# Performance work log

Measured on AMD Instinct MI355X. Metric: run time of the kernel, lower is better.

The kernel has to match this reference:

```python
import jax, jax.numpy as jnp
import numpy as np
from jax import lax

H = 64          # GRU hidden size
OUT_STEPS = 20  # output_seq_size


def _maxpool2(x):
    # x: [N, C, H, W] -> 2x2 max pool, stride 2, VALID
    return lax.reduce_window(x, -jnp.inf, lax.max, (1, 1, 2, 2), (1, 1, 2, 2), 'VALID')


def _conv(x, w, b):
    # NCHW / OIHW, VALID, stride 1
    y = lax.conv_general_dilated(x, w, (1, 1), 'VALID',
                                 dimension_numbers=('NCHW', 'OIHW', 'NCHW'))
    return y + b[None, :, None, None]


def _gru_step(h, x, wih, whh, bih, bhh):
    # PyTorch GRU gate order: r, z, n
    gi = x @ wih.T + bih            # [B, 3H]
    gh = h @ whh.T + bhh            # [B, 3H]
    i_r, i_z, i_n = jnp.split(gi, 3, axis=-1)
    h_r, h_z, h_n = jnp.split(gh, 3, axis=-1)
    r = jax.nn.sigmoid(i_r + h_r)
    z = jax.nn.sigmoid(i_z + h_z)
    n = jnp.tanh(i_n + r * h_n)
    return (1.0 - z) * n + z * h


def setup_inputs() -> dict:
    key = jax.random.key(0)
    ks = jax.random.split(key, 20)
    B, T = 1024, 31
    s = 0.1
    return {
        'bbox_seq': jax.random.normal(ks[0], (B, T, 4), jnp.float32),
        'head_seq': jax.random.uniform(ks[1], (B, T, 32, 32), jnp.float32),
        'conv1_w': jax.random.normal(ks[2], (4, 1, 3, 3), jnp.float32) * s,
        'conv1_b': jax.random.normal(ks[3], (4,), jnp.float32) * s,
        'conv2_w': jax.random.normal(ks[4], (10, 4, 3, 3), jnp.float32) * s,
        'conv2_b': jax.random.normal(ks[5], (10,), jnp.float32) * s,
        'fc_w': jax.random.normal(ks[6], (5, 360), jnp.float32) * s,
        'fc_b': jax.random.normal(ks[7], (5,), jnp.float32) * s,
        'enc_wih': jax.random.normal(ks[8], (3 * H, 9), jnp.float32) * s,
        'enc_whh': jax.random.normal(ks[9], (3 * H, H), jnp.float32) * s,
        'enc_bih': jax.random.normal(ks[10], (3 * H,), jnp.float32) * s,
        'enc_bhh': jax.random.normal(ks[11], (3 * H,), jnp.float32) * s,
        'dec_wih': jax.random.normal(ks[12], (3 * H, 4), jnp.float32) * s,
        'dec_whh': jax.random.normal(ks[13], (3 * H, H), jnp.float32) * s,
        'dec_bih': jax.random.normal(ks[14], (3 * H,), jnp.float32) * s,
        'dec_bhh': jax.random.normal(ks[15], (3 * H,), jnp.float32) * s,
        'lin_w': jax.random.normal(ks[16], (4, H), jnp.float32) * s,
        'lin_b': jax.random.normal(ks[17], (4,), jnp.float32) * s,
    }


def reference(bbox_seq, head_seq, conv1_w, conv1_b, conv2_w, conv2_b, fc_w, fc_b,
              enc_wih, enc_whh, enc_bih, enc_bhh,
              dec_wih, dec_whh, dec_bih, dec_bhh, lin_w, lin_b):
    B, T = bbox_seq.shape[0], bbox_seq.shape[1]
    L = T - 1  # encoder sequence length

    # offset: last bbox, broadcast over OUT_STEPS -> [B, OUT_STEPS, 4]
    offset = jnp.broadcast_to(bbox_seq[:, -1][:, None, :], (B, OUT_STEPS, 4))

    diffs = bbox_seq[:, 1:] - bbox_seq[:, :-1]  # [B, L, 4] (dropout p=0 -> identity)

    # --- ConvEncoder on all head crops at once ---
    imgs = head_seq[:, :-1].reshape(B * L, 1, 32, 32)
    x = jax.nn.relu(_conv(imgs, conv1_w, conv1_b))   # [BL, 4, 30, 30]
    x = _maxpool2(x)                                  # [BL, 4, 15, 15]
    x = jax.nn.relu(_conv(x, conv2_w, conv2_b))       # [BL, 10, 13, 13]
    x = _maxpool2(x)                                  # [BL, 10, 6, 6]
    emb = x.reshape(B * L, -1) @ fc_w.T + fc_b        # [BL, 5]
    emb = emb.reshape(B, L, -1)

    enc_in = jnp.concatenate([diffs, emb], axis=2)    # [B, L, 9]

    # --- GRU encoder (scan over time) ---
    def enc_step(h, x_t):
        h = _gru_step(h, x_t, enc_wih, enc_whh, enc_bih, enc_bhh)
        return h, None
    h0 = jnp.zeros((B, H), enc_in.dtype)
    hn, _ = lax.scan(enc_step, h0, jnp.swapaxes(enc_in, 0, 1))

    def dec_step(carry, _):
        h, prev_x = carry
        h = _gru_step(h, prev_x, dec_wih, dec_whh, dec_bih, dec_bhh)
        x_new = h @ lin_w.T + lin_b + prev_x
        return (h, x_new), x_new
    (_, _), outs = lax.scan(dec_step, (hn, diffs[:, -1]), None, length=OUT_STEPS)
    out = jnp.swapaxes(outs, 0, 1)                    # [B, OUT_STEPS, 4]

    return jnp.cumsum(out, axis=1) + offset
```

## Files before the change

### kernel.cpp

```cpp
#include <hip/hip_runtime.h>
#include <hip/hip_bf16.h>


#define B_    1024
#define L_    30
#define H_    64

__device__ __forceinline__ float sigmoid_f(float v) {
    return 1.f / (1.f + __expf(-v));
}
__device__ __forceinline__ float tanh_f(float v) {
    v = fminf(fmaxf(v, -15.f), 15.f);
    float e = __expf(2.f * v);
    return (e - 1.f) / (e + 1.f);
}
__device__ __forceinline__ float bcast(float v, int lane) {
    return __int_as_float(__builtin_amdgcn_readlane(__float_as_int(v), lane));
}
__device__ __forceinline__ void load4_lds(float* r, const float* p) {
    float2 a = *(const float2*)p;
    float2 b = *(const float2*)(p + 2);
    r[0] = a.x; r[1] = a.y; r[2] = b.x; r[3] = b.y;
}

__global__ __launch_bounds__(64) void conv_embed_kernel(
    const float* __restrict__ bbox,
    const float* __restrict__ head,
    const float* __restrict__ c1w, const float* __restrict__ c1b,
    const float* __restrict__ c2w, const float* __restrict__ c2b,
    const float* __restrict__ fcw, const float* __restrict__ fcb,
    float* __restrict__ enc_in)
{
    const int img = blockIdx.x;
    const int b = img / L_;
    const int l = img % L_;
    const int tid = threadIdx.x;

    __shared__ float s_img[32 * 32];
    __shared__ float s_p1[4 * 15 * 16];
    __shared__ float s_p2[360];
    __shared__ float s_red[60];

    {
        const float4* src = (const float4*)(head + ((size_t)b * 31 + (size_t)l) * 1024);
        float4* dst = (float4*)s_img;
        #pragma unroll
        for (int i = 0; i < 4; ++i) dst[tid + 64 * i] = src[tid + 64 * i];
    }
    __syncthreads();

    if (tid < 60) {
        const int c = tid / 15, px = tid % 15;
        const int x0 = 2 * px;
        float w[9];
        #pragma unroll
        for (int k = 0; k < 9; ++k) w[k] = c1w[c * 9 + k];
        const float bias = c1b[c];

        float r0[4], r1[4], r2[4], r3[4];
        load4_lds(r0, s_img + 0 * 32 + x0);
        load4_lds(r1, s_img + 1 * 32 + x0);
        #pragma unroll
        for (int py = 0; py < 15; ++py) {
            load4_lds(r2, s_img + (2 * py + 2) * 32 + x0);
            load4_lds(r3, s_img + (2 * py + 3) * 32 + x0);
            float a00 = bias, a01 = bias, a10 = bias, a11 = bias;
            #pragma unroll
            for (int kx = 0; kx < 3; ++kx) {
                const float w0 = w[kx], w1 = w[3 + kx], w2 = w[6 + kx];
                a00 = fmaf(w0, r0[kx],     fmaf(w1, r1[kx],     fmaf(w2, r2[kx],     a00)));
                a01 = fmaf(w0, r0[kx + 1], fmaf(w1, r1[kx + 1], fmaf(w2, r2[kx + 1], a01)));
                a10 = fmaf(w0, r1[kx],     fmaf(w1, r2[kx],     fmaf(w2, r3[kx],     a10)));
                a11 = fmaf(w0, r1[kx + 1], fmaf(w1, r2[kx + 1], fmaf(w2, r3[kx + 1], a11)));
            }
            a00 = fmaxf(a00, 0.f); a01 = fmaxf(a01, 0.f);
            a10 = fmaxf(a10, 0.f); a11 = fmaxf(a11, 0.f);
            s_p1[c * 240 + py * 16 + px] = fmaxf(fmaxf(a00, a01), fmaxf(a10, a11));
            #pragma unroll
            for (int q = 0; q < 4; ++q) { r0[q] = r2[q]; r1[q] = r3[q]; }
        }
    }
    __syncthreads();

    if (tid < 60) {
        const int c = tid / 6, px = tid % 6;
        const int x0 = 2 * px;
        float w[4][9];
        #pragma unroll
        for (int ic = 0; ic < 4; ++ic)
            #pragma unroll
            for (int k = 0; k < 9; ++k) w[ic][k] = c2w[(c * 4 + ic) * 9 + k];
        const float bias = c2b[c];

        float win[4][4][4];
        #pragma unroll
        for (int ic = 0; ic < 4; ++ic) {
            load4_lds(win[0][ic], s_p1 + ic * 240 + 0 * 16 + x0);
            load4_lds(win[1][ic], s_p1 + ic * 240 + 1 * 16 + x0);
        }
        #pragma unroll
        for (int py = 0; py < 6; ++py) {
            #pragma unroll
            for (int ic = 0; ic < 4; ++ic) {
                load4_lds(win[2][ic], s_p1 + ic * 240 + (2 * py + 2) * 16 + x0);
                load4_lds(win[3][ic], s_p1 + ic * 240 + (2 * py + 3) * 16 + x0);
            }
            float a00 = bias, a01 = bias, a10 = bias, a11 = bias;
            #pragma unroll
            for (int ic = 0; ic < 4; ++ic) {
                #pragma unroll
                for (int kx = 0; kx < 3; ++kx) {
                    const float w0 = w[ic][kx], w1 = w[ic][3 + kx], w2 = w[ic][6 + kx];
                    a00 = fmaf(w0, win[0][ic][kx],     fmaf(w1, win[1][ic][kx],     fmaf(w2, win[2][ic][kx],     a00)));
                    a01 = fmaf(w0, win[0][ic][kx + 1], fmaf(w1, win[1][ic][kx + 1], fmaf(w2, win[2][ic][kx + 1], a01)));
                    a10 = fmaf(w0, win[1][ic][kx],     fmaf(w1, win[2][ic][kx],     fmaf(w2, win[3][ic][kx],     a10)));
                    a11 = fmaf(w0, win[1][ic][kx + 1], fmaf(w1, win[2][ic][kx + 1], fmaf(w2, win[3][ic][kx + 1], a11)));
                }
            }
            a00 = fmaxf(a00, 0.f); a01 = fmaxf(a01, 0.f);
            a10 = fmaxf(a10, 0.f); a11 = fmaxf(a11, 0.f);
            s_p2[c * 36 + py * 6 + px] = fmaxf(fmaxf(a00, a01), fmaxf(a10, a11));
            #pragma unroll
            for (int ic = 0; ic < 4; ++ic)
                #pragma unroll
                for (int q = 0; q < 4; ++q) { win[0][ic][q] = win[2][ic][q]; win[1][ic][q] = win[3][ic][q]; }
        }
    }
    __syncthreads();

    if (tid < 60) {
        const int o = tid / 12, i0 = tid % 12;
        const float* wrow = fcw + o * 360;
        float acc = 0.f;
        #pragma unroll
        for (int k = 0; k < 30; ++k) {
            const int i = i0 + 12 * k;
            acc = fmaf(wrow[i], s_p2[i], acc);
        }
        s_red[tid] = acc;
    }
    __syncthreads();

    float* dst = enc_in + ((size_t)b * L_ + l) * 9;
    if (tid < 5) {
        float acc = fcb[tid];
        #pragma unroll
        for (int k = 0; k < 12; ++k) acc += s_red[tid * 12 + k];
        dst[4 + tid] = acc;
    } else if (tid >= 8 && tid < 12) {
        const int d = tid - 8;
        const float* bb = bbox + (size_t)b * 124 + (size_t)l * 4;
        dst[d] = bb[4 + d] - bb[d];
    }
}

__global__ __launch_bounds__(64, 1) void gru_encdec_kernel(
    const float* __restrict__ bbox,
    const float* __restrict__ enc_in,
    const float* __restrict__ ewih, const float* __restrict__ ewhh,
    const float* __restrict__ ebih, const float* __restrict__ ebhh,
    const float* __restrict__ dwih, const float* __restrict__ dwhh,
    const float* __restrict__ dbih, const float* __restrict__ dbhh,
    const float* __restrict__ linw, const float* __restrict__ linb,
    float* __restrict__ out)
{
    const int b = blockIdx.x;
    const int j = threadIdx.x;

    __shared__ float xs[272];
    for (int i = j; i < 270; i += 64) xs[i] = enc_in[(size_t)b * 270 + i];

    float h = 0.f;

    {
        float Wh[3][64];
        #pragma unroll
        for (int g = 0; g < 3; ++g) {
            const float4* row = (const float4*)(ewhh + (size_t)(g * 64 + j) * 64);
            #pragma unroll
            for (int k4 = 0; k4 < 16; ++k4) *(float4*)&Wh[g][4 * k4] = row[k4];
        }
        float Wi[3][9];
        #pragma unroll
        for (int g = 0; g < 3; ++g) {
            const float* row = ewih + (g * 64 + j) * 9;
            #pragma unroll
            for (int k = 0; k < 9; ++k) Wi[g][k] = row[k];
        }
        const float bi0 = ebih[j], bi1 = ebih[64 + j], bi2 = ebih[128 + j];
        const float bh0 = ebhh[j], bh1 = ebhh[64 + j], bh2 = ebhh[128 + j];

        __syncthreads();

        #pragma unroll 1
        for (int t = 0; t < L_; ++t) {
            float gr = bi0 + bh0, gz = bi1 + bh1, gni = bi2, gnh = bh2;
            #pragma unroll
            for (int k = 0; k < 9; ++k) {
                const float xk = xs[t * 9 + k];
                gr  = fmaf(Wi[0][k], xk, gr);
                gz  = fmaf(Wi[1][k], xk, gz);
                gni = fmaf(Wi[2][k], xk, gni);
            }
            #pragma unroll
            for (int k = 0; k < 64; ++k) {
                const float hk = bcast(h, k);
                gr  = fmaf(Wh[0][k], hk, gr);
                gz  = fmaf(Wh[1][k], hk, gz);
                gnh = fmaf(Wh[2][k], hk, gnh);
            }
            const float r = sigmoid_f(gr);
            const float z = sigmoid_f(gz);
            const float n = tanh_f(gni + r * gnh);
            h = (1.f - z) * n + z * h;
        }
    }

    {
        float Wh[3][64];
        #pragma unroll
        for (int g = 0; g < 3; ++g) {
            const float4* row = (const float4*)(dwhh + (size_t)(g * 64 + j) * 64);
            #pragma unroll
            for (int k4 = 0; k4 < 16; ++k4) *(float4*)&Wh[g][4 * k4] = row[k4];
        }
        float Wi[3][4];
        #pragma unroll
        for (int g = 0; g < 3; ++g) {
            const float* row = dwih + (g * 64 + j) * 4;
            #pragma unroll
            for (int k = 0; k < 4; ++k) Wi[g][k] = row[k];
        }
        const float bi0 = dbih[j], bi1 = dbih[64 + j], bi2 = dbih[128 + j];
        const float bh0 = dbhh[j], bh1 = dbhh[64 + j], bh2 = dbhh[128 + j];
        const float lw0 = linw[j], lw1 = linw[64 + j], lw2 = linw[128 + j], lw3 = linw[192 + j];
        const float lb0 = linb[0], lb1 = linb[1], lb2 = linb[2], lb3 = linb[3];

        const float* bb = bbox + (size_t)b * 124;
        float px0 = bb[120] - bb[116];
        float px1 = bb[121] - bb[117];
        float px2 = bb[122] - bb[118];
        float px3 = bb[123] - bb[119];
        const float of0 = bb[120], of1 = bb[121], of2 = bb[122], of3 = bb[123];
        float cs0 = 0.f, cs1 = 0.f, cs2 = 0.f, cs3 = 0.f;
        float4* outp = (float4*)(out + (size_t)b * 80);

        #pragma unroll 1
        for (int t = 0; t < 20; ++t) {
            float gr = bi0 + bh0, gz = bi1 + bh1, gni = bi2, gnh = bh2;
            gr  = fmaf(Wi[0][0], px0, fmaf(Wi[0][1], px1, fmaf(Wi[0][2], px2, fmaf(Wi[0][3], px3, gr))));
            gz  = fmaf(Wi[1][0], px0, fmaf(Wi[1][1], px1, fmaf(Wi[1][2], px2, fmaf(Wi[1][3], px3, gz))));
            gni = fmaf(Wi[2][0], px0, fmaf(Wi[2][1], px1, fmaf(Wi[2][2], px2, fmaf(Wi[2][3], px3, gni))));
            #pragma unroll
            for (int k = 0; k < 64; ++k) {
                const float hk = bcast(h, k);
                gr  = fmaf(Wh[0][k], hk, gr);
                gz  = fmaf(Wh[1][k], hk, gz);
                gnh = fmaf(Wh[2][k], hk, gnh);
            }
            const float r = sigmoid_f(gr);
            const float z = sigmoid_f(gz);
            const float n = tanh_f(gni + r * gnh);
            h = (1.f - z) * n + z * h;

            float v0 = lw0 * h, v1 = lw1 * h, v2 = lw2 * h, v3 = lw3 * h;
            #pragma unroll
            for (int s = 32; s > 0; s >>= 1) {
                v0 += __shfl_xor(v0, s);
                v1 += __shfl_xor(v1, s);
                v2 += __shfl_xor(v2, s);
                v3 += __shfl_xor(v3, s);
            }
            px0 = v0 + lb0 + px0;
            px1 = v1 + lb1 + px1;
            px2 = v2 + lb2 + px2;
            px3 = v3 + lb3 + px3;
            cs0 += px0; cs1 += px1; cs2 += px2; cs3 += px3;
            if (j == 0) outp[t] = make_float4(cs0 + of0, cs1 + of1, cs2 + of2, cs3 + of3);
        }
    }
}

extern "C" void kernel_launch(void* const* d_in, const int* in_sizes, int n_in,
                              void* d_out, int out_size, void* d_ws, size_t ws_size,
                              hipStream_t stream) {
    (void)in_sizes; (void)n_in; (void)out_size; (void)ws_size;
    const float* bbox = (const float*)d_in[0];
    const float* head = (const float*)d_in[1];
    const float* c1w  = (const float*)d_in[2];
    const float* c1b  = (const float*)d_in[3];
    const float* c2w  = (const float*)d_in[4];
    const float* c2b  = (const float*)d_in[5];
    const float* fcw  = (const float*)d_in[6];
    const float* fcb  = (const float*)d_in[7];
    const float* ewih = (const float*)d_in[8];
    const float* ewhh = (const float*)d_in[9];
    const float* ebih = (const float*)d_in[10];
    const float* ebhh = (const float*)d_in[11];
    const float* dwih = (const float*)d_in[12];
    const float* dwhh = (const float*)d_in[13];
    const float* dbih = (const float*)d_in[14];
    const float* dbhh = (const float*)d_in[15];
    const float* linw = (const float*)d_in[16];
    const float* linb = (const float*)d_in[17];
    float* out = (float*)d_out;

    float* enc_in = (float*)d_ws;

    conv_embed_kernel<<<B_ * L_, 64, 0, stream>>>(bbox, head, c1w, c1b, c2w, c2b,
                                                  fcw, fcb, enc_in);
    gru_encdec_kernel<<<B_, 64, 0, stream>>>(bbox, enc_in,
                                             ewih, ewhh, ebih, ebhh,
                                             dwih, dwhh, dbih, dbhh,
                                             linw, linb, out);
}
```

Baseline: 320.4 us.

## Use fp16 packed dot products for GRU recurrence and rotate conv row buffers

The GRU encoder and decoder recurrent weights are now held as packed half2 registers. The hidden state is broadcast through LDS as fp16 instead of 64 readlane operations, and v_dot2 fp16 instructions accumulate into fp32. This halves the register footprint of the weights and cuts the number of FMAs and broadcasts per step on the serial critical path, at the cost of reduced precision in the recurrence. Separately, the conv1 and conv2 loops use a 6-slot ring buffer of rows so that register copies between iterations are avoided.

```diff
diff --git a/kernel.cpp b/kernel.cpp
--- a/kernel.cpp
+++ b/kernel.cpp
@@ -5,6 +5,9 @@
 #define B_    1024
 #define L_    30
 #define H_    64
+
+typedef _Float16 half_t;
+typedef __attribute__((ext_vector_type(2))) _Float16 half2_t;
 
 __device__ __forceinline__ float sigmoid_f(float v) {
     return 1.f / (1.f + __expf(-v));
@@ -13,9 +16,6 @@
     v = fminf(fmaxf(v, -15.f), 15.f);
     float e = __expf(2.f * v);
     return (e - 1.f) / (e + 1.f);
-}
-__device__ __forceinline__ float bcast(float v, int lane) {
-    return __int_as_float(__builtin_amdgcn_readlane(__float_as_int(v), lane));
 }
 __device__ __forceinline__ void load4_lds(float* r, const float* p) {
     float2 a = *(const float2*)p;
@@ -52,78 +52,96 @@
     if (tid < 60) {
         const int c = tid / 15, px = tid % 15;
         const int x0 = 2 * px;
-        float w[9];
-        #pragma unroll
-        for (int k = 0; k < 9; ++k) w[k] = c1w[c * 9 + k];
+        float wg[9];
+        #pragma unroll
+        for (int k = 0; k < 9; ++k) wg[k] = c1w[c * 9 + k];
         const float bias = c1b[c];
 
-        float r0[4], r1[4], r2[4], r3[4];
-        load4_lds(r0, s_img + 0 * 32 + x0);
-        load4_lds(r1, s_img + 1 * 32 + x0);
-        #pragma unroll
-        for (int py = 0; py < 15; ++py) {
-            load4_lds(r2, s_img + (2 * py + 2) * 32 + x0);
-            load4_lds(r3, s_img + (2 * py + 3) * 32 + x0);
+        auto c1out = [&](const float* ra, const float* rb, const float* rc, const float* rd) -> float {
             float a00 = bias, a01 = bias, a10 = bias, a11 = bias;
             #pragma unroll
             for (int kx = 0; kx < 3; ++kx) {
-                const float w0 = w[kx], w1 = w[3 + kx], w2 = w[6 + kx];
-                a00 = fmaf(w0, r0[kx],     fmaf(w1, r1[kx],     fmaf(w2, r2[kx],     a00)));
-                a01 = fmaf(w0, r0[kx + 1], fmaf(w1, r1[kx + 1], fmaf(w2, r2[kx + 1], a01)));
-                a10 = fmaf(w0, r1[kx],     fmaf(w1, r2[kx],     fmaf(w2, r3[kx],     a10)));
-                a11 = fmaf(w0, r1[kx + 1], fmaf(w1, r2[kx + 1], fmaf(w2, r3[kx + 1], a11)));
+                const float w0 = wg[kx], w1 = wg[3 + kx], w2 = wg[6 + kx];
+                a00 = fmaf(w0, ra[kx],     fmaf(w1, rb[kx],     fmaf(w2, rc[kx],     a00)));
+                a01 = fmaf(w0, ra[kx + 1], fmaf(w1, rb[kx + 1], fmaf(w2, rc[kx + 1], a01)));
+                a10 = fmaf(w0, rb[kx],     fmaf(w1, rc[kx],     fmaf(w2, rd[kx],     a10)));
+                a11 = fmaf(w0, rb[kx + 1], fmaf(w1, rc[kx + 1], fmaf(w2, rd[kx + 1], a11)));
             }
             a00 = fmaxf(a00, 0.f); a01 = fmaxf(a01, 0.f);
             a10 = fmaxf(a10, 0.f); a11 = fmaxf(a11, 0.f);
-            s_p1[c * 240 + py * 16 + px] = fmaxf(fmaxf(a00, a01), fmaxf(a10, a11));
-            #pragma unroll
-            for (int q = 0; q < 4; ++q) { r0[q] = r2[q]; r1[q] = r3[q]; }
-        }
+            return fmaxf(fmaxf(a00, a01), fmaxf(a10, a11));
+        };
+
+        float r[6][4];
+        load4_lds(r[0], s_img + 0 * 32 + x0);
+        load4_lds(r[1], s_img + 1 * 32 + x0);
+        #pragma unroll
+        for (int i = 0; i < 7; ++i) {
+            const int s0 = (4 * i) % 6, s1 = (4 * i + 1) % 6, s2 = (4 * i + 2) % 6;
+            const int s3 = (4 * i + 3) % 6, s4 = (4 * i + 4) % 6, s5 = (4 * i + 5) % 6;
+            load4_lds(r[s2], s_img + (4 * i + 2) * 32 + x0);
+            load4_lds(r[s3], s_img + (4 * i + 3) * 32 + x0);
+            s_p1[c * 240 + (2 * i) * 16 + px] = c1out(r[s0], r[s1], r[s2], r[s3]);
+            load4_lds(r[s4], s_img + (4 * i + 4) * 32 + x0);
+            load4_lds(r[s5], s_img + (4 * i + 5) * 32 + x0);
+            s_p1[c * 240 + (2 * i + 1) * 16 + px] = c1out(r[s2], r[s3], r[s4], r[s5]);
+        }
+        load4_lds(r[0], s_img + 30 * 32 + x0);
+        load4_lds(r[1], s_img + 31 * 32 + x0);
+        s_p1[c * 240 + 14 * 16 + px] = c1out(r[4], r[5], r[0], r[1]);
     }
     __syncthreads();
 
     if (tid < 60) {
         const int c = tid / 6, px = tid % 6;
         const int x0 = 2 * px;
-        float w[4][9];
+        float wg2[4][9];
         #pragma unroll
         for (int ic = 0; ic < 4; ++ic)
             #pragma unroll
-            for (int k = 0; k < 9; ++k) w[ic][k] = c2w[(c * 4 + ic) * 9 + k];
-        const float bias = c2b[c];
-
-        float win[4][4][4];
-        #pragma unroll
-        for (int ic = 0; ic < 4; ++ic) {
-            load4_lds(win[0][ic], s_p1 + ic * 240 + 0 * 16 + x0);
-            load4_lds(win[1][ic], s_p1 + ic * 240 + 1 * 16 + x0);
-        }
-        #pragma unroll
-        for (int py = 0; py < 6; ++py) {
-            #pragma unroll
-            for (int ic = 0; ic < 4; ++ic) {
-                load4_lds(win[2][ic], s_p1 + ic * 240 + (2 * py + 2) * 16 + x0);
-                load4_lds(win[3][ic], s_p1 + ic * 240 + (2 * py + 3) * 16 + x0);
-            }
-            float a00 = bias, a01 = bias, a10 = bias, a11 = bias;
+            for (int k = 0; k < 9; ++k) wg2[ic][k] = c2w[(c * 4 + ic) * 9 + k];
+        const float bias2 = c2b[c];
+
+        float P[6][4][4];
+        auto c2out = [&](float (*pa)[4], float (*pb)[4], float (*pc)[4], float (*pd)[4]) -> float {
+            float a00 = bias2, a01 = bias2, a10 = bias2, a11 = bias2;
             #pragma unroll
             for (int ic = 0; ic < 4; ++ic) {
                 #pragma unroll
                 for (int kx = 0; kx < 3; ++kx) {
-                    const float w0 = w[ic][kx], w1 = w[ic][3 + kx], w2 = w[ic][6 + kx];
-                    a00 = fmaf(w0, win[0][ic][kx],     fmaf(w1, win[1][ic][kx],     fmaf(w2, win[2][ic][kx],     a00)));
-                    a01 = fmaf(w0, win[0][ic][kx + 1], fmaf(w1, win[1][ic][kx + 1], fmaf(w2, win[2][ic][kx + 1], a01)));
-                    a10 = fmaf(w0, win[1][ic][kx],     fmaf(w1, win[2][ic][kx],     fmaf(w2, win[3][ic][kx],     a10)));
-                    a11 = fmaf(w0, win[1][ic][kx + 1], fmaf(w1, win[2][ic][kx + 1], fmaf(w2, win[3][ic][kx + 1], a11)));
+                    const float w0 = wg2[ic][kx], w1 = wg2[ic][3 + kx], w2 = wg2[ic][6 + kx];
+                    a00 = fmaf(w0, pa[ic][kx],     fmaf(w1, pb[ic][kx],     fmaf(w2, pc[ic][kx],     a00)));
+                    a01 = fmaf(w0, pa[ic][kx + 1], fmaf(w1, pb[ic][kx + 1], fmaf(w2, pc[ic][kx + 1], a01)));
+                    a10 = fmaf(w0, pb[ic][kx],     fmaf(w1, pc[ic][kx],     fmaf(w2, pd[ic][kx],     a10)));
+                    a11 = fmaf(w0, pb[ic][kx + 1], fmaf(w1, pc[ic][kx + 1], fmaf(w2, pd[ic][kx + 1], a11)));
                 }
             }
             a00 = fmaxf(a00, 0.f); a01 = fmaxf(a01, 0.f);
             a10 = fmaxf(a10, 0.f); a11 = fmaxf(a11, 0.f);
-            s_p2[c * 36 + py * 6 + px] = fmaxf(fmaxf(a00, a01), fmaxf(a10, a11));
-            #pragma unroll
-            for (int ic = 0; ic < 4; ++ic)
-                #pragma unroll
-                for (int q = 0; q < 4; ++q) { win[0][ic][q] = win[2][ic][q]; win[1][ic][q] = win[3][ic][q]; }
+            return fmaxf(fmaxf(a00, a01), fmaxf(a10, a11));
+        };
+
+        #pragma unroll
+        for (int ic = 0; ic < 4; ++ic) {
+            load4_lds(P[0][ic], s_p1 + ic * 240 + 0 * 16 + x0);
+            load4_lds(P[1][ic], s_p1 + ic * 240 + 1 * 16 + x0);
+        }
+        #pragma unroll
+        for (int i = 0; i < 3; ++i) {
+            const int s0 = (4 * i) % 6, s1 = (4 * i + 1) % 6, s2 = (4 * i + 2) % 6;
+            const int s3 = (4 * i + 3) % 6, s4 = (4 * i + 4) % 6, s5 = (4 * i + 5) % 6;
+            #pragma unroll
+            for (int ic = 0; ic < 4; ++ic) {
+                load4_lds(P[s2][ic], s_p1 + ic * 240 + (4 * i + 2) * 16 + x0);
+                load4_lds(P[s3][ic], s_p1 + ic * 240 + (4 * i + 3) * 16 + x0);
+            }
+            s_p2[c * 36 + (2 * i) * 6 + px] = c2out(P[s0], P[s1], P[s2], P[s3]);
+            #pragma unroll
+            for (int ic = 0; ic < 4; ++ic) {
+                load4_lds(P[s4][ic], s_p1 + ic * 240 + (4 * i + 4) * 16 + x0);
+                load4_lds(P[s5][ic], s_p1 + ic * 240 + (4 * i + 5) * 16 + x0);
+            }
+            s_p2[c * 36 + (2 * i + 1) * 6 + px] = c2out(P[s2], P[s3], P[s4], P[s5]);
         }
     }
     __syncthreads();
@@ -167,18 +185,24 @@
     const int b = blockIdx.x;
     const int j = threadIdx.x;
 
-    __shared__ float xs[272];
+    __shared__ float  xs[272];
+    __shared__ half_t hs[64];
+
     for (int i = j; i < 270; i += 64) xs[i] = enc_in[(size_t)b * 270 + i];
 
     float h = 0.f;
 
     {
-        float Wh[3][64];
+        half2_t Wh2[3][32];
         #pragma unroll
         for (int g = 0; g < 3; ++g) {
             const float4* row = (const float4*)(ewhh + (size_t)(g * 64 + j) * 64);
             #pragma unroll
-            for (int k4 = 0; k4 < 16; ++k4) *(float4*)&Wh[g][4 * k4] = row[k4];
+            for (int k4 = 0; k4 < 16; ++k4) {
+                const float4 v = row[k4];
+                Wh2[g][2 * k4]     = half2_t{(half_t)v.x, (half_t)v.y};
+                Wh2[g][2 * k4 + 1] = half2_t{(half_t)v.z, (half_t)v.w};
+            }
         }
         float Wi[3][9];
         #pragma unroll
@@ -194,6 +218,9 @@
 
         #pragma unroll 1
         for (int t = 0; t < L_; ++t) {
+            hs[j] = (half_t)h;
+            __builtin_amdgcn_wave_barrier();
+
             float gr = bi0 + bh0, gz = bi1 + bh1, gni = bi2, gnh = bh2;
             #pragma unroll
             for (int k = 0; k < 9; ++k) {
@@ -202,27 +229,33 @@
                 gz  = fmaf(Wi[1][k], xk, gz);
                 gni = fmaf(Wi[2][k], xk, gni);
             }
-            #pragma unroll
-            for (int k = 0; k < 64; ++k) {
-                const float hk = bcast(h, k);
-                gr  = fmaf(Wh[0][k], hk, gr);
-                gz  = fmaf(Wh[1][k], hk, gz);
-                gnh = fmaf(Wh[2][k], hk, gnh);
+            const half2_t* hp = (const half2_t*)hs;
+            #pragma unroll
+            for (int k2 = 0; k2 < 32; ++k2) {
+                const half2_t h2 = hp[k2];
+                gr  = __builtin_amdgcn_fdot2(Wh2[0][k2], h2, gr,  false);
+                gz  = __builtin_amdgcn_fdot2(Wh2[1][k2], h2, gz,  false);
+                gnh = __builtin_amdgcn_fdot2(Wh2[2][k2], h2, gnh, false);
             }
             const float r = sigmoid_f(gr);
             const float z = sigmoid_f(gz);
             const float n = tanh_f(gni + r * gnh);
             h = (1.f - z) * n + z * h;
+            __builtin_amdgcn_wave_barrier();
         }
     }
 
     {
-        float Wh[3][64];
+        half2_t Wh2[3][32];
         #pragma unroll
         for (int g = 0; g < 3; ++g) {
             const float4* row = (const float4*)(dwhh + (size_t)(g * 64 + j) * 64);
             #pragma unroll
-            for (int k4 = 0; k4 < 16; ++k4) *(float4*)&Wh[g][4 * k4] = row[k4];
+            for (int k4 = 0; k4 < 16; ++k4) {
+                const float4 v = row[k4];
+                Wh2[g][2 * k4]     = half2_t{(half_t)v.x, (half_t)v.y};
+                Wh2[g][2 * k4 + 1] = half2_t{(half_t)v.z, (half_t)v.w};
+            }
         }
         float Wi[3][4];
         #pragma unroll
@@ -247,21 +280,27 @@
 
         #pragma unroll 1
         for (int t = 0; t < 20; ++t) {
+            hs[j] = (half_t)h;
+            __builtin_amdgcn_wave_barrier();
+
             float gr = bi0 + bh0, gz = bi1 + bh1, gni = bi2, gnh = bh2;
             gr  = fmaf(Wi[0][0], px0, fmaf(Wi[0][1], px1, fmaf(Wi[0][2], px2, fmaf(Wi[0][3], px3, gr))));
             gz  = fmaf(Wi[1][0], px0, fmaf(Wi[1][1], px1, fmaf(Wi[1][2], px2, fmaf(Wi[1][3], px3, gz))));
             gni = fmaf(Wi[2][0], px0, fmaf(Wi[2][1], px1, fmaf(Wi[2][2], px2, fmaf(Wi[2][3], px3, gni))));
-            #pragma unroll
-            for (int k = 0; k < 64; ++k) {
-                const float hk = bcast(h, k);
-                gr  = fmaf(Wh[0][k], hk, gr);
-                gz  = fmaf(Wh[1][k], hk, gz);
-                gnh = fmaf(Wh[2][k], hk, gnh);
+
+            const half2_t* hp = (const half2_t*)hs;
+            #pragma unroll
+            for (int k2 = 0; k2 < 32; ++k2) {
+                const half2_t h2 = hp[k2];
+                gr  = __builtin_amdgcn_fdot2(Wh2[0][k2], h2, gr,  false);
+                gz  = __builtin_amdgcn_fdot2(Wh2[1][k2], h2, gz,  false);
+                gnh = __builtin_amdgcn_fdot2(Wh2[2][k2], h2, gnh, false);
             }
             const float r = sigmoid_f(gr);
             const float z = sigmoid_f(gz);
             const float n = tanh_f(gni + r * gnh);
             h = (1.f - z) * n + z * h;
+            __builtin_amdgcn_wave_barrier();
 
             float v0 = lw0 * h, v1 = lw1 * h, v2 = lw2 * h, v3 = lw3 * h;
             #pragma unroll
```

Result: faster. 298.3 us (-6.9%).
